# Kernel tuning notes

Measured on AMD Instinct MI355X. Metric: run time of the kernel, lower is better.

Reference implementation:

```python
import jax, jax.numpy as jnp
import numpy as np

EPS = 1e-5  # torch BatchNorm2d default eps
K = 3       # kernel_size
D = 1       # dilation (== padding)


def setup_inputs() -> dict:
    key = jax.random.key(0)
    k0, k1, k2 = jax.random.split(key, 3)
    N, C, H, W, O = 4, 2048, 32, 32, 256
    return {
        "x": jax.random.normal(k0, (N, C, H, W), jnp.float32),
        "conv_w": jax.random.normal(k1, (K * K, C, K, K), jnp.float32) * 0.01,
        "gamma": jnp.ones((K * K,), jnp.float32),
        "beta": jnp.zeros((K * K,), jnp.float32),
        "weight": jax.random.normal(k2, (O, C, K * K), jnp.float32) * 0.01,
    }


def reference(x, conv_w, gamma, beta, weight):
    n, c, h, w = x.shape
    # --- dynamic-kernel generator: conv (stride 1, pad=dilation) -> BN (train mode) -> softmax over K*K ---
    sigma = jax.lax.conv_general_dilated(
        x, conv_w, window_strides=(1, 1), padding=[(D, D), (D, D)],
        rhs_dilation=(D, D), dimension_numbers=("NCHW", "OIHW", "NCHW"))  # (n, K*K, h, w)
    mean = sigma.mean(axis=(0, 2, 3), keepdims=True)
    var = sigma.var(axis=(0, 2, 3), keepdims=True)  # biased variance, as torch BN uses for normalization
    sigma = (sigma - mean) * jax.lax.rsqrt(var + EPS)
    sigma = sigma * gamma[None, :, None, None] + beta[None, :, None, None]
    sigma = jax.nn.softmax(sigma, axis=1)            # softmax over the K*K kernel positions
    sigma = sigma.reshape(n, K * K, h * w)           # (n, K*K, h*w)
    # --- unfold (im2col), channel-major (C, kh, kw) ordering matching torch F.unfold ---
    patches = jax.lax.conv_general_dilated_patches(
        x, (K, K), (1, 1), [(D, D), (D, D)], rhs_dilation=(D, D),
        dimension_numbers=("NCHW", "OIHW", "NCHW"))  # (n, C*K*K, h, w)
    patches = patches.reshape(n, c, K * K, h * w)     # (n, C, K*K, h*w)
    # --- per-pixel dynamic weighting + learned projection ---
    # out[n,o,m] = sum_{c,l} patches[n,c,l,m] * sigma[n,l,m] * weight[o,c,l]
    out = jnp.einsum("nclm,nlm,ocl->nom", patches, sigma, weight)
    return out.reshape(n, weight.shape[0], h, w)
```

## Files before the change

kernel.cpp:

```cpp
#include <hip/hip_runtime.h>
#include <hip/hip_bf16.h>
#include <stdint.h>

typedef unsigned short u16;
typedef __attribute__((ext_vector_type(8))) short short8;
typedef __attribute__((ext_vector_type(4))) float floatx4;

#define N_IMG 4
#define C_IN  2048
#define HW    1024
#define KK    9
#define O_OUT 256
#define NPIX  4096
#define M_PAD  2432
#define K_DIM  2048
#define BN_EPS 1e-5f

#define OFF_A    0u
#define OFF_XT   9961472u
#define OFF_H    26738688u
#define OFF_SRAW 46661632u
#define OFF_STAT 46809088u

__device__ __forceinline__ u16 f2b(float f) {
    unsigned u = __float_as_uint(f);
    return (u16)((u + 0x7FFFu + ((u >> 16) & 1u)) >> 16);
}

__device__ __forceinline__ void load8f(const float* base, size_t eidx, u16* out) {
    const float* p = base + eidx;
    float4 a = ((const float4*)p)[0];
    float4 b = ((const float4*)p)[1];
    float f[8] = {a.x, a.y, a.z, a.w, b.x, b.y, b.z, b.w};
#pragma unroll
    for (int j = 0; j < 8; ++j) out[j] = f2b(f[j]);
}

__global__ void build_all(const float* __restrict__ x, const float* __restrict__ wgt,
                          const float* __restrict__ cw, u16* __restrict__ xt,
                          u16* __restrict__ A, float* __restrict__ stats) {
    __shared__ __align__(16) u16 lds[9 * 2056];
    int b = blockIdx.x, t = threadIdx.x;
    if (b < 2048) {
        int c0 = (b & 31) * 64, p0 = ((b >> 5) & 15) * 64, n = b >> 9;
        int r = t >> 3, pv = (t & 7) * 8;
        u16 h0[8], h1[8];
        load8f(x, (size_t)(n * C_IN + c0 + r) * HW + p0 + pv, h0);
        load8f(x, (size_t)(n * C_IN + c0 + r + 32) * HW + p0 + pv, h1);
#pragma unroll
        for (int j = 0; j < 8; ++j) {
            lds[(pv + j) * 72 + r]      = h0[j];
            lds[(pv + j) * 72 + r + 32] = h1[j];
        }
        __syncthreads();
        int pr = t >> 3, cv = (t & 7) * 8;
        uint4 o0 = *(const uint4*)&lds[pr * 72 + cv];
        uint4 o1 = *(const uint4*)&lds[(pr + 32) * 72 + cv];
        *(uint4*)(xt + (size_t)(n * HW + p0 + pr) * K_DIM + c0 + cv) = o0;
        *(uint4*)(xt + (size_t)(n * HW + p0 + pr + 32) * K_DIM + c0 + cv) = o1;
    } else if (b < 2304) {
        int o = b - 2048;
        size_t base = (size_t)o * 18432;
        for (int i = 0; i < 9; ++i) {
            int e0 = (t + i * 256) * 8;
            u16 hv[8];
            load8f(wgt, base + e0, hv);
#pragma unroll
            for (int j = 0; j < 8; ++j) {
                int e = e0 + j;
                int c = e / 9, l = e - c * 9;
                lds[l * 2056 + c] = hv[j];
            }
        }
        __syncthreads();
        for (int l = 0; l < 9; ++l) {
            size_t row = (size_t)l * 256 + o;
            *(uint4*)(A + row * K_DIM + t * 8) = *(const uint4*)&lds[l * 2056 + t * 8];
        }
    } else if (b < 2313) {
        int l = b - 2304;
        size_t base = (size_t)l * 18432;
        for (int i = 0; i < 9; ++i) {
            int e0 = (t + i * 256) * 8;
            u16 hv[8];
            load8f(cw, base + e0, hv);
#pragma unroll
            for (int j = 0; j < 8; ++j) {
                int e = e0 + j;
                int c = e / 9, k = e - c * 9;
                lds[k * 2056 + c] = hv[j];
            }
        }
        __syncthreads();
        for (int k = 0; k < 9; ++k) {
            size_t row = 2304 + (size_t)k * 9 + l;
            *(uint4*)(A + row * K_DIM + t * 8) = *(const uint4*)&lds[k * 2056 + t * 8];
        }
    } else {
        uint4 z = {0, 0, 0, 0};
        uint4* dst = (uint4*)(A + (size_t)2385 * K_DIM);
        for (int i = t; i < (47 * 2048) / 8; i += 256) dst[i] = z;
        if (t < 18) stats[t] = 0.0f;
    }
}

__device__ __forceinline__ void gload_lds16(const void* g, void* l) {
    __builtin_amdgcn_global_load_lds((__attribute__((address_space(1))) void*)(g),
                                     (__attribute__((address_space(3))) void*)(l), 16, 0, 0);
}

__global__ void gemm_bt(const u16* __restrict__ A, const u16* __restrict__ B,
                        __hip_bfloat16* __restrict__ C) {
    __shared__ __align__(16) u16 As[2 * 128 * 32];
    __shared__ __align__(16) u16 Bs[2 * 128 * 32];
    int bx = blockIdx.x;
    int mt = bx % 19, nt = bx / 19;
    int m0 = mt * 128, n0 = nt * 128;
    int t = threadIdx.x;
    int w = t >> 6, lam = t & 63;
    int wm = w >> 1, wn = w & 1;
    int lm = lam & 15, q = lam >> 4;

    floatx4 acc[4][4];
    floatx4 z = {0.f, 0.f, 0.f, 0.f};
#pragma unroll
    for (int i = 0; i < 4; ++i)
#pragma unroll
        for (int j = 0; j < 4; ++j) acc[i][j] = z;

    int rsub = lam >> 2;
    int kc = (lam & 3) * 8;
    const u16* gA[4]; const u16* gB[4];
    u16* lA[4];       u16* lB[4];
#pragma unroll
    for (int ii = 0; ii < 4; ++ii) {
        int c = w * 4 + ii;
        int rc = c & 7, ks = c >> 3;
        gA[ii] = A + (size_t)(m0 + rc * 16 + rsub) * K_DIM + ks * 32 + kc;
        gB[ii] = B + (size_t)(n0 + rc * 16 + rsub) * K_DIM + ks * 32 + kc;
        lA[ii] = As + ks * 4096 + rc * 512;
        lB[ii] = Bs + ks * 4096 + rc * 512;
    }

    for (int kt = 0; kt < K_DIM / 64; ++kt) {
#pragma unroll
        for (int ii = 0; ii < 4; ++ii) {
            gload_lds16(gA[ii], lA[ii]);
            gload_lds16(gB[ii], lB[ii]);
            gA[ii] += 64; gB[ii] += 64;
        }
        __syncthreads();
#pragma unroll
        for (int ks = 0; ks < 2; ++ks) {
            short8 af[4], bf[4];
#pragma unroll
            for (int i = 0; i < 4; ++i)
                af[i] = *(const short8*)(As + ks * 4096 + (wm * 64 + i * 16 + lm) * 32 + q * 8);
#pragma unroll
            for (int j = 0; j < 4; ++j)
                bf[j] = *(const short8*)(Bs + ks * 4096 + (wn * 64 + j * 16 + lm) * 32 + q * 8);
#pragma unroll
            for (int i = 0; i < 4; ++i)
#pragma unroll
                for (int j = 0; j < 4; ++j)
                    acc[i][j] = __builtin_amdgcn_mfma_f32_16x16x32_bf16(af[i], bf[j], acc[i][j], 0, 0, 0);
        }
        __syncthreads();
    }
#pragma unroll
    for (int i = 0; i < 4; ++i) {
        int gm = m0 + wm * 64 + i * 16 + q * 4;
#pragma unroll
        for (int j = 0; j < 4; ++j) {
            int gn = n0 + wn * 64 + j * 16 + lm;
#pragma unroll
            for (int r = 0; r < 4; ++r)
                C[(size_t)(gm + r) * NPIX + gn] = __float2bfloat16(acc[i][j][r]);
        }
    }
}

__global__ void sigma_stats(const __hip_bfloat16* __restrict__ Hm, float* __restrict__ sraw,
                            float* __restrict__ stats) {
    int b = blockIdx.x;
    int qq = b & 3, nl = b >> 2;
    int n = nl / 9, l = nl - n * 9;
    int t = threadIdx.x;
    int pix = qq * 256 + t;
    int y = pix >> 5, x = pix & 31;
    float v = 0.f;
#pragma unroll
    for (int k = 0; k < 9; ++k) {
        int yy = y + k / 3 - 1, xx = x + (k % 3) - 1;
        if (yy >= 0 && yy < 32 && xx >= 0 && xx < 32)
            v += __bfloat162float(Hm[(size_t)(2304 + k * 9 + l) * NPIX + n * HW + yy * 32 + xx]);
    }
    sraw[(size_t)nl * HW + pix] = v;
    __shared__ float r1[256], r2[256];
    r1[t] = v; r2[t] = v * v;
    __syncthreads();
    for (int s = 128; s > 0; s >>= 1) {
        if (t < s) { r1[t] += r1[t + s]; r2[t] += r2[t + s]; }
        __syncthreads();
    }
    if (t == 0) { atomicAdd(&stats[l], r1[0]); atomicAdd(&stats[9 + l], r2[0]); }
}

__global__ void tail(const __hip_bfloat16* __restrict__ Hm, const float* __restrict__ sraw,
                     const float* __restrict__ stats, const float* __restrict__ gamma,
                     const float* __restrict__ beta, float* __restrict__ out) {
    int b = blockIdx.x;
    int n = b >> 8, o = b & 255;
    int t = threadIdx.x;
    float mean[9], istd[9], gg[9], bb[9];
#pragma unroll
    for (int l = 0; l < 9; ++l) {
        float m = stats[l] * (1.f / 4096.f);
        float var = stats[9 + l] * (1.f / 4096.f) - m * m;
        mean[l] = m; istd[l] = rsqrtf(var + BN_EPS);
        gg[l] = gamma[l]; bb[l] = beta[l];
    }
    for (int i = 0; i < 4; ++i) {
        int pix = t + i * 256;
        int y = pix >> 5, x = pix & 31;
        float v[9];
        float mx = -1e30f;
#pragma unroll
        for (int l = 0; l < 9; ++l) {
            float tv = (sraw[(size_t)(n * 9 + l) * HW + pix] - mean[l]) * istd[l];
            tv = tv * gg[l] + bb[l];
            v[l] = tv; mx = fmaxf(mx, tv);
        }
        float ssum = 0.f;
#pragma unroll
        for (int l = 0; l < 9; ++l) { v[l] = __expf(v[l] - mx); ssum += v[l]; }
        float inv = 1.f / ssum;
        float acc = 0.f;
#pragma unroll
        for (int l = 0; l < 9; ++l) {
            int dy = l / 3 - 1, dx = l % 3 - 1;
            int yy = y + dy, xx = x + dx;
            if (yy >= 0 && yy < 32 && xx >= 0 && xx < 32) {
                float h = __bfloat162float(Hm[(size_t)(l * 256 + o) * NPIX + n * HW + yy * 32 + xx]);
                acc += v[l] * inv * h;
            }
        }
        out[((size_t)n * 256 + o) * HW + pix] = acc;
    }
}

extern "C" void kernel_launch(void* const* d_in, const int* in_sizes, int n_in,
                              void* d_out, int out_size, void* d_ws, size_t ws_size,
                              hipStream_t stream) {
    const float* x     = (const float*)d_in[0];
    const float* cw    = (const float*)d_in[1];
    const float* gamma = (const float*)d_in[2];
    const float* beta  = (const float*)d_in[3];
    const float* wgt   = (const float*)d_in[4];

    char* ws = (char*)d_ws;
    u16*   Abuf = (u16*)(ws + OFF_A);
    u16*   XT   = (u16*)(ws + OFF_XT);
    u16*   Hm   = (u16*)(ws + OFF_H);
    float* sraw = (float*)(ws + OFF_SRAW);
    float* stats= (float*)(ws + OFF_STAT);

    build_all<<<2314, 256, 0, stream>>>(x, wgt, cw, XT, Abuf, stats);
    gemm_bt<<<19 * 32, 256, 0, stream>>>(Abuf, XT, (__hip_bfloat16*)Hm);
    sigma_stats<<<N_IMG * KK * 4, 256, 0, stream>>>((const __hip_bfloat16*)Hm, sraw, stats);
    tail<<<N_IMG * O_OUT, 256, 0, stream>>>((const __hip_bfloat16*)Hm, sraw, stats, gamma, beta, (float*)d_out);
}
```

Measured before the change: 175.9 us.

## Pack transpose LDS writes as 32-bit pairs and give tail threads 4 pixels by 2 outputs

In the x-transpose part of build_all, two adjacent channels are packed into one 32-bit LDS word with a padded stride of 35. This halves the LDS store count and is meant to cut bank conflicts. The tail kernel now gives each thread 4 consecutive pixels and 2 output channels, with sraw loaded as float4 and the results written with float4 stores. The grid shrinks from 1024 to 512 blocks, so the softmax work is shared across two outputs and memory accesses are wider, at the cost of more registers and fewer blocks.

```diff
diff --git a/kernel.cpp b/kernel.cpp
--- a/kernel.cpp
+++ b/kernel.cpp
@@ -43,21 +43,25 @@
     int b = blockIdx.x, t = threadIdx.x;
     if (b < 2048) {
         int c0 = (b & 31) * 64, p0 = ((b >> 5) & 15) * 64, n = b >> 9;
-        int r = t >> 3, pv = (t & 7) * 8;
+        int rp = t >> 3;
+        int pv = (t & 7) * 8;
         u16 h0[8], h1[8];
-        load8f(x, (size_t)(n * C_IN + c0 + r) * HW + p0 + pv, h0);
-        load8f(x, (size_t)(n * C_IN + c0 + r + 32) * HW + p0 + pv, h1);
-#pragma unroll
-        for (int j = 0; j < 8; ++j) {
-            lds[(pv + j) * 72 + r]      = h0[j];
-            lds[(pv + j) * 72 + r + 32] = h1[j];
-        }
-        __syncthreads();
-        int pr = t >> 3, cv = (t & 7) * 8;
-        uint4 o0 = *(const uint4*)&lds[pr * 72 + cv];
-        uint4 o1 = *(const uint4*)&lds[(pr + 32) * 72 + cv];
-        *(uint4*)(xt + (size_t)(n * HW + p0 + pr) * K_DIM + c0 + cv) = o0;
-        *(uint4*)(xt + (size_t)(n * HW + p0 + pr + 32) * K_DIM + c0 + cv) = o1;
+        load8f(x, (size_t)(n * C_IN + c0 + 2 * rp) * HW + p0 + pv, h0);
+        load8f(x, (size_t)(n * C_IN + c0 + 2 * rp + 1) * HW + p0 + pv, h1);
+        unsigned* l32 = (unsigned*)lds;
+#pragma unroll
+        for (int j = 0; j < 8; ++j)
+            l32[(pv + j) * 35 + rp] = (unsigned)h0[j] | ((unsigned)h1[j] << 16);
+        __syncthreads();
+        int pr = t >> 3, cq = (t & 7) * 4;
+        unsigned o0[4], o1[4];
+#pragma unroll
+        for (int i = 0; i < 4; ++i) {
+            o0[i] = l32[pr * 35 + cq + i];
+            o1[i] = l32[(pr + 32) * 35 + cq + i];
+        }
+        *(uint4*)(xt + (size_t)(n * HW + p0 + pr) * K_DIM + c0 + cq * 2) = *(uint4*)o0;
+        *(uint4*)(xt + (size_t)(n * HW + p0 + pr + 32) * K_DIM + c0 + cq * 2) = *(uint4*)o1;
     } else if (b < 2304) {
         int o = b - 2048;
         size_t base = (size_t)o * 18432;
@@ -210,7 +214,7 @@
                      const float* __restrict__ stats, const float* __restrict__ gamma,
                      const float* __restrict__ beta, float* __restrict__ out) {
     int b = blockIdx.x;
-    int n = b >> 8, o = b & 255;
+    int n = b >> 7, og = b & 127;
     int t = threadIdx.x;
     float mean[9], istd[9], gg[9], bb[9];
 #pragma unroll
@@ -220,14 +224,28 @@
         mean[l] = m; istd[l] = rsqrtf(var + BN_EPS);
         gg[l] = gamma[l]; bb[l] = beta[l];
     }
-    for (int i = 0; i < 4; ++i) {
-        int pix = t + i * 256;
-        int y = pix >> 5, x = pix & 31;
+    int pix0 = t * 4;
+    int y = pix0 >> 5, x0 = pix0 & 31;
+    float sr[9][4];
+#pragma unroll
+    for (int l = 0; l < 9; ++l)
+        *(float4*)sr[l] = *(const float4*)&sraw[(size_t)(n * 9 + l) * HW + pix0];
+
+    float acc0[4], acc1[4];
+#pragma unroll
+    for (int j = 0; j < 4; ++j) { acc0[j] = 0.f; acc1[j] = 0.f; }
+
+    const __hip_bfloat16* hb = Hm + (size_t)n * HW;
+    size_t obase = (size_t)(og * 2) * NPIX;
+
+#pragma unroll
+    for (int j = 0; j < 4; ++j) {
+        int x = x0 + j;
         float v[9];
         float mx = -1e30f;
 #pragma unroll
         for (int l = 0; l < 9; ++l) {
-            float tv = (sraw[(size_t)(n * 9 + l) * HW + pix] - mean[l]) * istd[l];
+            float tv = (sr[l][j] - mean[l]) * istd[l];
             tv = tv * gg[l] + bb[l];
             v[l] = tv; mx = fmaxf(mx, tv);
         }
@@ -235,18 +253,21 @@
 #pragma unroll
         for (int l = 0; l < 9; ++l) { v[l] = __expf(v[l] - mx); ssum += v[l]; }
         float inv = 1.f / ssum;
-        float acc = 0.f;
 #pragma unroll
         for (int l = 0; l < 9; ++l) {
             int dy = l / 3 - 1, dx = l % 3 - 1;
             int yy = y + dy, xx = x + dx;
             if (yy >= 0 && yy < 32 && xx >= 0 && xx < 32) {
-                float h = __bfloat162float(Hm[(size_t)(l * 256 + o) * NPIX + n * HW + yy * 32 + xx]);
-                acc += v[l] * inv * h;
+                float sv = v[l] * inv;
+                size_t hidx = (size_t)l * 256 * NPIX + obase + (size_t)(pix0 + j + dy * 32 + dx);
+                acc0[j] += sv * __bfloat162float(hb[hidx]);
+                acc1[j] += sv * __bfloat162float(hb[hidx + NPIX]);
             }
         }
-        out[((size_t)n * 256 + o) * HW + pix] = acc;
-    }
+    }
+    float* ob = out + ((size_t)n * 256 + og * 2) * HW + pix0;
+    *(float4*)ob = *(float4*)acc0;
+    *(float4*)(ob + HW) = *(float4*)acc1;
 }
 
 extern "C" void kernel_launch(void* const* d_in, const int* in_sizes, int n_in,
@@ -268,5 +289,5 @@
     build_all<<<2314, 256, 0, stream>>>(x, wgt, cw, XT, Abuf, stats);
     gemm_bt<<<19 * 32, 256, 0, stream>>>(Abuf, XT, (__hip_bfloat16*)Hm);
     sigma_stats<<<N_IMG * KK * 4, 256, 0, stream>>>((const __hip_bfloat16*)Hm, sraw, stats);
-    tail<<<N_IMG * O_OUT, 256, 0, stream>>>((const __hip_bfloat16*)Hm, sraw, stats, gamma, beta, (float*)d_out);
-}
+    tail<<<512, 256, 0, stream>>>((const __hip_bfloat16*)Hm, sraw, stats, gamma, beta, (float*)d_out);
+}
```

Result: faster. 172.0 us (-2.2%).
